# Optimization experiments

Measured on AMD Instinct MI355X. Metric: run time of the kernel, lower is better.

## Reference

```python
import jax, jax.numpy as jnp
import numpy as np

INPUT, HIDDEN, OUTPUT, LAYERS = 256, 512, 256, 2


def _lstm_cell(x, h, c, Wih, Whh, bih, bhh):
    # gates in torch order: i, f, g, o  -> [B, 4H]
    g = x @ Wih.T + bih + h @ Whh.T + bhh
    i, f, gg, o = jnp.split(g, 4, axis=-1)
    c_new = jax.nn.sigmoid(f) * c + jax.nn.sigmoid(i) * jnp.tanh(gg)
    h_new = jax.nn.sigmoid(o) * jnp.tanh(c_new)
    return h_new, c_new


def setup_inputs() -> dict:
    key = jax.random.key(0)
    ks = jax.random.split(key, 16)
    s = 0.05
    inp = {
        "z0": jax.random.normal(ks[0], (1024, INPUT), jnp.float32),
        "h0": jax.random.normal(ks[1], (LAYERS, 1024, HIDDEN), jnp.float32),
        "c0": jax.random.normal(ks[2], (LAYERS, 1024, HIDDEN), jnp.float32),
        # layer 0: input_size -> hidden
        "W_ih0": jax.random.normal(ks[3], (4 * HIDDEN, INPUT), jnp.float32) * s,
        "W_hh0": jax.random.normal(ks[4], (4 * HIDDEN, HIDDEN), jnp.float32) * s,
        "b_ih0": jax.random.normal(ks[5], (4 * HIDDEN,), jnp.float32) * s,
        "b_hh0": jax.random.normal(ks[6], (4 * HIDDEN,), jnp.float32) * s,
        # layer 1: hidden -> hidden
        "W_ih1": jax.random.normal(ks[7], (4 * HIDDEN, HIDDEN), jnp.float32) * s,
        "W_hh1": jax.random.normal(ks[8], (4 * HIDDEN, HIDDEN), jnp.float32) * s,
        "b_ih1": jax.random.normal(ks[9], (4 * HIDDEN,), jnp.float32) * s,
        "b_hh1": jax.random.normal(ks[10], (4 * HIDDEN,), jnp.float32) * s,
        # fc: hidden -> input (feedback), linear: input -> output
        "fc_W": jax.random.normal(ks[11], (INPUT, HIDDEN), jnp.float32) * s,
        "fc_b": jax.random.normal(ks[12], (INPUT,), jnp.float32) * s,
        "lin_W": jax.random.normal(ks[13], (OUTPUT, INPUT), jnp.float32) * s,
        "lin_b": jax.random.normal(ks[14], (OUTPUT,), jnp.float32) * s,
        "T2": 128,
    }
    return inp


def reference(z0, h0, c0, W_ih0, W_hh0, b_ih0, b_hh0,
              W_ih1, W_hh1, b_ih1, b_hh1, fc_W, fc_b, lin_W, lin_b, T2):
    params = [(W_ih0, W_hh0, b_ih0, b_hh0), (W_ih1, W_hh1, b_ih1, b_hh1)]

    def step(carry, _):
        z, h, c = carry          # z:[B,in], h/c:[L,B,H]
        x = z
        hs, cs = [], []
        for l, (Wih, Whh, bih, bhh) in enumerate(params):
            hn, cn = _lstm_cell(x, h[l], c[l], Wih, Whh, bih, bhh)
            hs.append(hn); cs.append(cn)
            x = hn
        z_new = x @ fc_W.T + fc_b
        return (z_new, jnp.stack(hs), jnp.stack(cs)), z_new

    _, zs = jax.lax.scan(step, (z0, h0, c0), None, length=T2)  # [T2,B,in]
    return zs @ lin_W.T + lin_b  # [T2, B, output]
```

## Files before the change

kernel.cpp:

```cpp
#include <hip/hip_runtime.h>


typedef __attribute__((ext_vector_type(8))) __bf16 bf16x8;
typedef __attribute__((ext_vector_type(16))) float f32x16;
typedef unsigned long long ull;

__device__ __forceinline__ f32x16 mfma_bf16(bf16x8 a, bf16x8 b, f32x16 c) {
  return __builtin_amdgcn_mfma_f32_32x32x16_bf16(a, b, c, 0, 0, 0);
}

__device__ __forceinline__ short f2bf(float f) {
  unsigned u = __float_as_uint(f);
  u += 0x7fffu + ((u >> 16) & 1u);
  return (short)(u >> 16);
}

__device__ __forceinline__ float sigm(float x) { return 1.0f / (1.0f + __expf(-x)); }
__device__ __forceinline__ float tanh_fast(float x) { return 2.0f / (1.0f + __expf(-2.0f * x)) - 1.0f; }

__device__ __forceinline__ f32x16 zero16() {
  f32x16 z;
#pragma unroll
  for (int i = 0; i < 16; ++i) z[i] = 0.0f;
  return z;
}

__device__ __forceinline__ void dma16(const void* g, void* l) {
  __builtin_amdgcn_global_load_lds(
      (const __attribute__((address_space(1))) void*)g,
      (__attribute__((address_space(3))) void*)l, 16, 0, 0);
}

#define AT_STRIDE 132

__global__ __launch_bounds__(256) void prep_kernel(
    const float* __restrict__ z0, const float* __restrict__ h0in,
    const float* __restrict__ Wih0, const float* __restrict__ Whh0,
    const float* __restrict__ bih0, const float* __restrict__ bhh0,
    const float* __restrict__ Wih1, const float* __restrict__ Whh1,
    const float* __restrict__ bih1, const float* __restrict__ bhh1,
    const float* __restrict__ fcW, const float* __restrict__ linW,
    short* __restrict__ wsw0, short* __restrict__ wsw1,
    short* __restrict__ fcWsw, short* __restrict__ linWsw,
    float* __restrict__ bias0, float* __restrict__ bias1,
    short* __restrict__ zb1, short* __restrict__ h0b0, short* __restrict__ h1b0,
    int* __restrict__ flags)
{
  int idx = blockIdx.x * 256 + threadIdx.x;
  if (idx < 1572864) {
    int jj = idx & 7, l = (idx >> 3) & 63, gg = (idx >> 9) & 3;
    int rest = idx >> 11;
    int s = rest % 48, b = rest / 48;
    int row = gg * 512 + b * 32 + (l & 31);
    int k = s * 16 + (l >> 5) * 8 + jj;
    wsw0[idx] = f2bf(k < 256 ? Wih0[row * 256 + k] : Whh0[row * 512 + (k - 256)]);
    return;
  }
  idx -= 1572864;
  if (idx < 2097152) {
    int jj = idx & 7, l = (idx >> 3) & 63, gg = (idx >> 9) & 3;
    int rest = idx >> 11;
    int s = rest & 63, b = rest >> 6;
    int row = gg * 512 + b * 32 + (l & 31);
    int k = s * 16 + (l >> 5) * 8 + jj;
    wsw1[idx] = f2bf(k < 512 ? Wih1[row * 512 + k] : Whh1[row * 512 + (k - 512)]);
    return;
  }
  idx -= 2097152;
  if (idx < 131072) {
    int jj = idx & 7, l = (idx >> 3) & 63, s = (idx >> 9) & 31, jz = idx >> 14;
    int col = jz * 32 + (l & 31);
    int k = s * 16 + (l >> 5) * 8 + jj;
    fcWsw[idx] = f2bf(fcW[col * 512 + k]);
    return;
  }
  idx -= 131072;
  if (idx < 65536) {
    int jj = idx & 7, l = (idx >> 3) & 63, s = (idx >> 9) & 15, jo = idx >> 13;
    int col = jo * 32 + (l & 31);
    int k = s * 16 + (l >> 5) * 8 + jj;
    linWsw[idx] = f2bf(linW[col * 256 + k]);
    return;
  }
  idx -= 65536;
  if (idx < 2048) { bias0[idx] = bih0[idx] + bhh0[idx]; return; }
  idx -= 2048;
  if (idx < 2048) { bias1[idx] = bih1[idx] + bhh1[idx]; return; }
  idx -= 2048;
  if (idx < 262144) { zb1[idx] = f2bf(z0[idx]); return; }
  idx -= 262144;
  if (idx < 524288) { h0b0[idx] = f2bf(h0in[idx]); return; }
  idx -= 524288;
  if (idx < 524288) { h1b0[idx] = f2bf(h0in[524288 + idx]); return; }
  idx -= 524288;
  if (idx < 8448) {
    int v = 0;
    if (idx < 8192) {
      int off = idx & 255;
      if (off == 32) v = 8;
      else if (off == 64 || off == 128) v = 16;
    }
    flags[idx] = v;
    return;
  }
}

__device__ __forceinline__ void wait1(int* c0, int v0) {
  __syncthreads();
  if (threadIdx.x == 0) {
    while (__hip_atomic_load(c0, __ATOMIC_RELAXED, __HIP_MEMORY_SCOPE_AGENT) < v0)
      __builtin_amdgcn_s_sleep(2);
    asm volatile("buffer_inv" ::: "memory");
  }
  __syncthreads();
}

__device__ __forceinline__ void wait2(int* c0, int v0, int* c1, int v1) {
  __syncthreads();
  if (threadIdx.x == 0) {
    while (__hip_atomic_load(c0, __ATOMIC_RELAXED, __HIP_MEMORY_SCOPE_AGENT) < v0 ||
           __hip_atomic_load(c1, __ATOMIC_RELAXED, __HIP_MEMORY_SCOPE_AGENT) < v1)
      __builtin_amdgcn_s_sleep(2);
    asm volatile("buffer_inv" ::: "memory");
  }
  __syncthreads();
}

__device__ __forceinline__ void produce(int* c) {
  asm volatile("s_waitcnt vmcnt(0)" ::: "memory");
  __syncthreads();
  if (threadIdx.x == 0)
    __hip_atomic_fetch_add(c, 1, __ATOMIC_RELAXED, __HIP_MEMORY_SCOPE_AGENT);
}

__device__ __forceinline__ void cell_warm(short* Bl, const short* __restrict__ wgl) {
  __syncthreads();
  const int t = threadIdx.x, w = t >> 6;
#pragma unroll
  for (int g = 0; g < 5; ++g)
#pragma unroll
    for (int i = 0; i < 2; ++i)
      dma16(wgl + (size_t)g * 8192 + (i * 512 + t) * 8,
            Bl + g * 8192 + i * 4096 + w * 512);
}

template <int NG, int TAG>
__device__ __forceinline__ void cell_phase_dma(
    short* Al, short* Bl, float* gbuf,
    const short* __restrict__ srcA, int ldA,
    const short* __restrict__ srcB, int ldB,
    const short* __restrict__ wgl,
    const float* __restrict__ bias,
    float* cr, short* hout, int row0, int j0)
{
  const int t = threadIdx.x;
  const int w = t >> 6, l = t & 63;
  const int gq = w >> 1, mh = w & 1;
  const int ln = l & 31, kh = l >> 5;

  auto issueA = [&](int g) {
    const short* asrc; int ald, gk;
    if (g < TAG) { asrc = srcA; ald = ldA; gk = g * 64; }
    else         { asrc = srcB; ald = ldB; gk = (g - TAG) * 64; }
    const short* gp = asrc + (size_t)(row0 + l) * ald + gk + w * 8;
    dma16(gp, Al + (g % 3) * 4096 + w * 512);
  };
  auto issueB = [&](int g) {
    const short* gb = wgl + (size_t)g * 8192;
    short* lb = Bl + (g % 5) * 8192;
#pragma unroll
    for (int i = 0; i < 2; ++i)
      dma16(gb + (i * 512 + t) * 8, lb + i * 4096 + w * 512);
  };

  f32x16 acc = zero16();
  issueA(0); issueA(1); issueA(2);

#pragma unroll
  for (int g = 0; g < NG; ++g) {
    if (g == 0)          asm volatile("s_waitcnt vmcnt(2)" ::: "memory");
    else if (g == 1)     asm volatile("s_waitcnt vmcnt(4)" ::: "memory");
    else if (g == 2)     asm volatile("s_waitcnt vmcnt(6)" ::: "memory");
    else if (g + 4 < NG) asm volatile("s_waitcnt vmcnt(8)" ::: "memory");
    else if (g + 3 < NG) asm volatile("s_waitcnt vmcnt(6)" ::: "memory");
    else if (g + 2 < NG) asm volatile("s_waitcnt vmcnt(4)" ::: "memory");
    else if (g + 1 < NG) asm volatile("s_waitcnt vmcnt(1)" ::: "memory");
    else                 asm volatile("s_waitcnt vmcnt(0)" ::: "memory");
    __builtin_amdgcn_s_barrier();
    __builtin_amdgcn_sched_barrier(0);
    const short* al = Al + (g % 3) * 4096;
    const short* bl = Bl + (g % 5) * 8192;
#pragma unroll
    for (int u = 0; u < 4; ++u) {
      bf16x8 a = *(const bf16x8*)&al[((u * 2 + kh) * 64 + mh * 32 + ln) * 8];
      bf16x8 b = *(const bf16x8*)&bl[((u * 4 + gq) * 64 + l) * 8];
      acc = mfma_bf16(a, b, acc);
    }
    __builtin_amdgcn_sched_barrier(0);
    __builtin_amdgcn_s_barrier();
    __builtin_amdgcn_sched_barrier(0);
    if (g + 3 < NG) issueA(g + 3);
    if (g + 5 < NG) issueB(g + 5);
  }

#pragma unroll
  for (int r = 0; r < 16; ++r) {
    int mloc = (r & 3) + 8 * (r >> 2) + 4 * kh + mh * 32;
    gbuf[(gq * 64 + mloc) * 32 + ln] = acc[r];
  }
  __syncthreads();
  const int m = t >> 3, nb = (t & 7) * 4;
  short hh[4];
#pragma unroll
  for (int u = 0; u < 4; ++u) {
    int n = nb + u, jn = j0 + n;
    float gi = gbuf[(0 * 64 + m) * 32 + n] + bias[jn];
    float gf = gbuf[(1 * 64 + m) * 32 + n] + bias[512 + jn];
    float gg = gbuf[(2 * 64 + m) * 32 + n] + bias[1024 + jn];
    float go = gbuf[(3 * 64 + m) * 32 + n] + bias[1536 + jn];
    float cn = sigm(gf) * cr[u] + sigm(gi) * tanh_fast(gg);
    cr[u] = cn;
    hh[u] = f2bf(sigm(go) * tanh_fast(cn));
  }
  ull hv; __builtin_memcpy(&hv, hh, 8);
  *(ull*)&hout[(size_t)(row0 + m) * 512 + j0 + nb] = hv;
}

template <int NQ>
__device__ __forceinline__ void proj_partials(
    short* At0, float* gbuf,
    const short* __restrict__ src, int ld,
    const short* __restrict__ wblk, int row0)
{
  const int t = threadIdx.x;
  const int w = t >> 6, l = t & 63;
  const int kq = w >> 1, mh = w & 1;
  const int ln = l & 31, kh = l >> 5;
  const int sks = t & 15, sm = t >> 4;
  f32x16 acc = zero16();
  uint4 pre[NQ][2];
#pragma unroll
  for (int q = 0; q < NQ; ++q)
#pragma unroll
    for (int i = 0; i < 2; ++i)
      pre[q][i] = *(const uint4*)&src[(row0 + sm + 32 * i) * ld + q * 128 + sks * 8];
#pragma unroll
  for (int q = 0; q < NQ; ++q) {
    __syncthreads();
#pragma unroll
    for (int i = 0; i < 2; ++i)
      *(uint4*)&At0[(sm + 32 * i) * AT_STRIDE + sks * 8] = pre[q][i];
    __syncthreads();
#pragma unroll
    for (int sl = 0; sl < 2; ++sl) {
      int s16 = kq * 2 + sl;
      bf16x8 a = *(const bf16x8*)&At0[(mh * 32 + ln) * AT_STRIDE + (s16 * 2 + kh) * 8];
      bf16x8 b = *(const bf16x8*)&wblk[((q * 8 + s16) * 64 + l) * 8];
      acc = mfma_bf16(a, b, acc);
    }
  }
  __syncthreads();
#pragma unroll
  for (int r = 0; r < 16; ++r) {
    int mloc = (r & 3) + 8 * (r >> 2) + 4 * kh + mh * 32;
    gbuf[(kq * 64 + mloc) * 32 + ln] = acc[r];
  }
  __syncthreads();
}

__global__ __launch_bounds__(512, 1) void decoder_persist(
    const short* __restrict__ wsw0, const short* __restrict__ wsw1,
    const short* __restrict__ fcWsw, const short* __restrict__ linWsw,
    const float* __restrict__ bias0, const float* __restrict__ bias1,
    const float* __restrict__ fcb, const float* __restrict__ linb,
    const float* __restrict__ c0in,
    short* h0x, short* h0y, short* h1x, short* h1y, short* zx, short* zy,
    int* flags, float* __restrict__ outp)
{
  __shared__ __align__(16) short Al[12288];
  __shared__ __align__(16) short Bl[40960];
  __shared__ int sgj[2];
  float* gbuf = (float*)Bl;
  short* Atp = Bl;
  float* gbufp = (float*)(Bl + 8448);

  if (threadIdx.x == 0) {
    unsigned xcc;
    asm volatile("s_getreg_b32 %0, hwreg(HW_REG_XCC_ID, 0, 32)" : "=s"(xcc));
    xcc &= 7u;
    int slot = __hip_atomic_fetch_add(&flags[8192 + (int)xcc * 32], 1,
                                      __ATOMIC_RELAXED, __HIP_MEMORY_SCOPE_AGENT);
    slot &= 31;
    sgj[0] = (int)xcc * 2 + (slot >> 4);
    sgj[1] = slot & 15;
  }
  __syncthreads();
  const int g = sgj[0], j = sgj[1];
  const int row0 = g * 64, j0 = j * 32;
  int* cnt = &flags[g * 256];
#define CZ(i)  (cnt + (0 + (i)) * 32)
#define CH0(i) (cnt + (2 + (i)) * 32)
#define CH1(i) (cnt + (4 + (i)) * 32)

  float c0r[4], c1r[4];
  {
    const int m = threadIdx.x >> 3, nb = (threadIdx.x & 7) * 4;
#pragma unroll
    for (int u = 0; u < 4; ++u) {
      c0r[u] = c0in[(size_t)(row0 + m) * 512 + j0 + nb + u];
      c1r[u] = c0in[524288 + (size_t)(row0 + m) * 512 + j0 + nb + u];
    }
  }

  short* h0buf[2] = {h0x, h0y};
  short* h1buf[2] = {h1x, h1y};
  short* zbuf[2] = {zx, zy};
  const short* wg0 = wsw0 + j * 98304;
  const short* wg1 = wsw1 + j * 131072;
  const short* wpj = (j < 8) ? (fcWsw + j * 16384) : (linWsw + (j - 8) * 8192);

#pragma unroll 1
  for (int t = 0; t < 128; ++t) {
    const int p = t & 1;
    const int half = (t >> 1) + 1;
    const int full = (t + 3) >> 1;
    cell_warm(Bl, wg0);
    wait2(CZ(p ^ 1), 8 * half, CH0(p), 16 * half);
    cell_phase_dma<12, 4>(Al, Bl, gbuf, zbuf[p ^ 1], 256, h0buf[p], 512,
                          wg0, bias0, c0r, h0buf[p ^ 1], row0, j0);
    produce(CH0(p ^ 1));
    cell_warm(Bl, wg1);
    wait2(CH0(p ^ 1), 16 * full, CH1(p), 16 * half);
    cell_phase_dma<16, 8>(Al, Bl, gbuf, h0buf[p ^ 1], 512, h1buf[p], 512,
                          wg1, bias1, c1r, h1buf[p ^ 1], row0, j0);
    produce(CH1(p ^ 1));
    if (j < 8) {
      wait1(CH1(p ^ 1), 16 * full);
      proj_partials<4>(Atp, gbufp, h1buf[p ^ 1], 512, wpj, row0);
      const int m = threadIdx.x >> 3, nb = (threadIdx.x & 7) * 4;
      const int n0 = j * 32;
      short zz[4];
#pragma unroll
      for (int u = 0; u < 4; ++u) {
        int n = nb + u;
        float v = gbufp[(0 * 64 + m) * 32 + n] + gbufp[(1 * 64 + m) * 32 + n] +
                  gbufp[(2 * 64 + m) * 32 + n] + gbufp[(3 * 64 + m) * 32 + n] +
                  fcb[n0 + n];
        zz[u] = f2bf(v);
      }
      ull zv; __builtin_memcpy(&zv, zz, 8);
      *(ull*)&zbuf[p][(size_t)(row0 + m) * 256 + n0 + nb] = zv;
      produce(CZ(p));
    } else if (t > 0) {
      proj_partials<2>(Atp, gbufp, zbuf[p ^ 1], 256, wpj, row0);
      const int m = threadIdx.x >> 3, nb = (threadIdx.x & 7) * 4;
      const int n0 = (j - 8) * 32;
      float4 ov;
      float* po = &ov.x;
#pragma unroll
      for (int u = 0; u < 4; ++u) {
        int n = nb + u;
        po[u] = gbufp[(0 * 64 + m) * 32 + n] + gbufp[(1 * 64 + m) * 32 + n] +
                gbufp[(2 * 64 + m) * 32 + n] + gbufp[(3 * 64 + m) * 32 + n] +
                linb[n0 + n];
      }
      *(float4*)&outp[(size_t)(t - 1) * 262144 + (size_t)(row0 + m) * 256 + n0 + nb] = ov;
    }
  }
  if (j >= 8) {
    wait1(CZ(1), 8 * 65);
    proj_partials<2>(Atp, gbufp, zbuf[1], 256, wpj, row0);
    const int m = threadIdx.x >> 3, nb = (threadIdx.x & 7) * 4;
    const int n0 = (j - 8) * 32;
    float4 ov;
    float* po = &ov.x;
#pragma unroll
    for (int u = 0; u < 4; ++u) {
      int n = nb + u;
      po[u] = gbufp[(0 * 64 + m) * 32 + n] + gbufp[(1 * 64 + m) * 32 + n] +
              gbufp[(2 * 64 + m) * 32 + n] + gbufp[(3 * 64 + m) * 32 + n] +
              linb[n0 + n];
    }
    *(float4*)&outp[(size_t)127 * 262144 + (size_t)(row0 + m) * 256 + n0 + nb] = ov;
  }
#undef CZ
#undef CH0
#undef CH1
}

extern "C" void kernel_launch(void* const* d_in, const int* in_sizes, int n_in,
                              void* d_out, int out_size, void* d_ws, size_t ws_size,
                              hipStream_t stream) {
  const float* z0   = (const float*)d_in[0];
  const float* h0in = (const float*)d_in[1];
  const float* c0in = (const float*)d_in[2];
  const float* Wih0 = (const float*)d_in[3];
  const float* Whh0 = (const float*)d_in[4];
  const float* bih0 = (const float*)d_in[5];
  const float* bhh0 = (const float*)d_in[6];
  const float* Wih1 = (const float*)d_in[7];
  const float* Whh1 = (const float*)d_in[8];
  const float* bih1 = (const float*)d_in[9];
  const float* bhh1 = (const float*)d_in[10];
  const float* fcW  = (const float*)d_in[11];
  const float* fcb  = (const float*)d_in[12];
  const float* linW = (const float*)d_in[13];
  const float* linb = (const float*)d_in[14];
  float* out = (float*)d_out;

  char* ws = (char*)d_ws;
  short* wsw0  = (short*)(ws + 0);
  short* wsw1  = (short*)(ws + 3145728);
  short* fcWsw = (short*)(ws + 7340032);
  short* linWsw= (short*)(ws + 7602176);
  float* bias0 = (float*)(ws + 7733248);
  float* bias1 = (float*)(ws + 7741440);
  short* zb0   = (short*)(ws + 7749632);
  short* zb1   = (short*)(ws + 8273920);
  short* h0b0  = (short*)(ws + 8798208);
  short* h0b1  = (short*)(ws + 9846784);
  short* h1b0  = (short*)(ws + 10895360);
  short* h1b1  = (short*)(ws + 11943936);
  int*   flags = (int*)  (ws + 12992512);

  prep_kernel<<<20273, 256, 0, stream>>>(z0, h0in, Wih0, Whh0, bih0, bhh0,
                                         Wih1, Whh1, bih1, bhh1, fcW, linW,
                                         wsw0, wsw1, fcWsw, linWsw, bias0, bias1,
                                         zb1, h0b0, h1b0, flags);

  decoder_persist<<<256, 512, 0, stream>>>(
      wsw0, wsw1, fcWsw, linWsw, bias0, bias1, fcb, linb, c0in,
      h0b0, h0b1, h1b0, h1b1, zb0, zb1, flags, out);
}
```

Measured before the change: 4.820 ms.

## Reorder K to put recurrent state first and prefetch it before the cross-block wait

Swaps the weight packing so the recurrent hidden-state K range comes before the input range. The first three A tiles, which depend only on the block's own previous h, can then be DMA'd before waiting on the other blocks' flags. The weight ring deepens from 5 to 6 stages and LDS grows to match. Biases are hoisted into registers and projection weights are preloaded into registers. This hides latency on the serial recurrence critical path, at the cost of more LDS and registers and trickier vmcnt bookkeeping.

```diff
diff --git a/kernel.cpp b/kernel.cpp
--- a/kernel.cpp
+++ b/kernel.cpp
@@ -53,7 +53,7 @@
     int s = rest % 48, b = rest / 48;
     int row = gg * 512 + b * 32 + (l & 31);
     int k = s * 16 + (l >> 5) * 8 + jj;
-    wsw0[idx] = f2bf(k < 256 ? Wih0[row * 256 + k] : Whh0[row * 512 + (k - 256)]);
+    wsw0[idx] = f2bf(k < 512 ? Whh0[row * 512 + k] : Wih0[row * 256 + (k - 512)]);
     return;
   }
   idx -= 1572864;
@@ -63,7 +63,7 @@
     int s = rest & 63, b = rest >> 6;
     int row = gg * 512 + b * 32 + (l & 31);
     int k = s * 16 + (l >> 5) * 8 + jj;
-    wsw1[idx] = f2bf(k < 512 ? Wih1[row * 512 + k] : Whh1[row * 512 + (k - 512)]);
+    wsw1[idx] = f2bf(k < 512 ? Whh1[row * 512 + k] : Wih1[row * 512 + (k - 512)]);
     return;
   }
   idx -= 2097152;
@@ -137,11 +137,20 @@
   __syncthreads();
   const int t = threadIdx.x, w = t >> 6;
 #pragma unroll
-  for (int g = 0; g < 5; ++g)
+  for (int g = 0; g < 6; ++g)
 #pragma unroll
     for (int i = 0; i < 2; ++i)
       dma16(wgl + (size_t)g * 8192 + (i * 512 + t) * 8,
             Bl + g * 8192 + i * 4096 + w * 512);
+}
+
+__device__ __forceinline__ void proA3(short* Al, const short* __restrict__ srcA,
+                                      int ldA, int row0) {
+  const int t = threadIdx.x, w = t >> 6, l = t & 63;
+#pragma unroll
+  for (int g = 0; g < 3; ++g)
+    dma16(srcA + (size_t)(row0 + l) * ldA + g * 64 + w * 8,
+          Al + g * 4096 + w * 512);
 }
 
 template <int NG, int TAG>
@@ -150,7 +159,7 @@
     const short* __restrict__ srcA, int ldA,
     const short* __restrict__ srcB, int ldB,
     const short* __restrict__ wgl,
-    const float* __restrict__ bias,
+    const float (&br)[4][4],
     float* cr, short* hout, int row0, int j0)
 {
   const int t = threadIdx.x;
@@ -167,29 +176,29 @@
   };
   auto issueB = [&](int g) {
     const short* gb = wgl + (size_t)g * 8192;
-    short* lb = Bl + (g % 5) * 8192;
+    short* lb = Bl + (g % 6) * 8192;
 #pragma unroll
     for (int i = 0; i < 2; ++i)
       dma16(gb + (i * 512 + t) * 8, lb + i * 4096 + w * 512);
   };
 
   f32x16 acc = zero16();
-  issueA(0); issueA(1); issueA(2);
 
 #pragma unroll
   for (int g = 0; g < NG; ++g) {
-    if (g == 0)          asm volatile("s_waitcnt vmcnt(2)" ::: "memory");
-    else if (g == 1)     asm volatile("s_waitcnt vmcnt(4)" ::: "memory");
-    else if (g == 2)     asm volatile("s_waitcnt vmcnt(6)" ::: "memory");
-    else if (g + 4 < NG) asm volatile("s_waitcnt vmcnt(8)" ::: "memory");
-    else if (g + 3 < NG) asm volatile("s_waitcnt vmcnt(6)" ::: "memory");
-    else if (g + 2 < NG) asm volatile("s_waitcnt vmcnt(4)" ::: "memory");
-    else if (g + 1 < NG) asm volatile("s_waitcnt vmcnt(1)" ::: "memory");
-    else                 asm volatile("s_waitcnt vmcnt(0)" ::: "memory");
+    if (g == 0)           asm volatile("s_waitcnt vmcnt(2)" ::: "memory");
+    else if (g == 1)      asm volatile("s_waitcnt vmcnt(4)" ::: "memory");
+    else if (g == 2)      asm volatile("s_waitcnt vmcnt(6)" ::: "memory");
+    else if (g + 6 <= NG) asm volatile("s_waitcnt vmcnt(8)" ::: "memory");
+    else if (g + 5 == NG) asm volatile("s_waitcnt vmcnt(6)" ::: "memory");
+    else if (g + 4 == NG) asm volatile("s_waitcnt vmcnt(4)" ::: "memory");
+    else if (g + 3 == NG) asm volatile("s_waitcnt vmcnt(2)" ::: "memory");
+    else if (g + 2 == NG) asm volatile("s_waitcnt vmcnt(1)" ::: "memory");
+    else                  asm volatile("s_waitcnt vmcnt(0)" ::: "memory");
     __builtin_amdgcn_s_barrier();
     __builtin_amdgcn_sched_barrier(0);
     const short* al = Al + (g % 3) * 4096;
-    const short* bl = Bl + (g % 5) * 8192;
+    const short* bl = Bl + (g % 6) * 8192;
 #pragma unroll
     for (int u = 0; u < 4; ++u) {
       bf16x8 a = *(const bf16x8*)&al[((u * 2 + kh) * 64 + mh * 32 + ln) * 8];
@@ -200,7 +209,7 @@
     __builtin_amdgcn_s_barrier();
     __builtin_amdgcn_sched_barrier(0);
     if (g + 3 < NG) issueA(g + 3);
-    if (g + 5 < NG) issueB(g + 5);
+    if (g + 6 < NG) issueB(g + 6);
   }
 
 #pragma unroll
@@ -213,11 +222,11 @@
   short hh[4];
 #pragma unroll
   for (int u = 0; u < 4; ++u) {
-    int n = nb + u, jn = j0 + n;
-    float gi = gbuf[(0 * 64 + m) * 32 + n] + bias[jn];
-    float gf = gbuf[(1 * 64 + m) * 32 + n] + bias[512 + jn];
-    float gg = gbuf[(2 * 64 + m) * 32 + n] + bias[1024 + jn];
-    float go = gbuf[(3 * 64 + m) * 32 + n] + bias[1536 + jn];
+    int n = nb + u;
+    float gi = gbuf[(0 * 64 + m) * 32 + n] + br[0][u];
+    float gf = gbuf[(1 * 64 + m) * 32 + n] + br[1][u];
+    float gg = gbuf[(2 * 64 + m) * 32 + n] + br[2][u];
+    float go = gbuf[(3 * 64 + m) * 32 + n] + br[3][u];
     float cn = sigm(gf) * cr[u] + sigm(gi) * tanh_fast(gg);
     cr[u] = cn;
     hh[u] = f2bf(sigm(go) * tanh_fast(cn));
@@ -239,11 +248,16 @@
   const int sks = t & 15, sm = t >> 4;
   f32x16 acc = zero16();
   uint4 pre[NQ][2];
-#pragma unroll
-  for (int q = 0; q < NQ; ++q)
+  bf16x8 bfr[NQ][2];
+#pragma unroll
+  for (int q = 0; q < NQ; ++q) {
 #pragma unroll
     for (int i = 0; i < 2; ++i)
       pre[q][i] = *(const uint4*)&src[(row0 + sm + 32 * i) * ld + q * 128 + sks * 8];
+#pragma unroll
+    for (int sl = 0; sl < 2; ++sl)
+      bfr[q][sl] = *(const bf16x8*)&wblk[((q * 8 + kq * 2 + sl) * 64 + l) * 8];
+  }
 #pragma unroll
   for (int q = 0; q < NQ; ++q) {
     __syncthreads();
@@ -255,8 +269,7 @@
     for (int sl = 0; sl < 2; ++sl) {
       int s16 = kq * 2 + sl;
       bf16x8 a = *(const bf16x8*)&At0[(mh * 32 + ln) * AT_STRIDE + (s16 * 2 + kh) * 8];
-      bf16x8 b = *(const bf16x8*)&wblk[((q * 8 + s16) * 64 + l) * 8];
-      acc = mfma_bf16(a, b, acc);
+      acc = mfma_bf16(a, bfr[q][sl], acc);
     }
   }
   __syncthreads();
@@ -278,7 +291,7 @@
     int* flags, float* __restrict__ outp)
 {
   __shared__ __align__(16) short Al[12288];
-  __shared__ __align__(16) short Bl[40960];
+  __shared__ __align__(16) short Bl[49152];
   __shared__ int sgj[2];
   float* gbuf = (float*)Bl;
   short* Atp = Bl;
@@ -302,13 +315,20 @@
 #define CH0(i) (cnt + (2 + (i)) * 32)
 #define CH1(i) (cnt + (4 + (i)) * 32)
 
-  float c0r[4], c1r[4];
+  float c0r[4], c1r[4], b0r[4][4], b1r[4][4], fbr[4];
   {
     const int m = threadIdx.x >> 3, nb = (threadIdx.x & 7) * 4;
 #pragma unroll
     for (int u = 0; u < 4; ++u) {
       c0r[u] = c0in[(size_t)(row0 + m) * 512 + j0 + nb + u];
       c1r[u] = c0in[524288 + (size_t)(row0 + m) * 512 + j0 + nb + u];
+      int jn = j0 + nb + u;
+#pragma unroll
+      for (int gt = 0; gt < 4; ++gt) {
+        b0r[gt][u] = bias0[gt * 512 + jn];
+        b1r[gt][u] = bias1[gt * 512 + jn];
+      }
+      fbr[u] = (j < 8) ? fcb[j * 32 + nb + u] : linb[(j - 8) * 32 + nb + u];
     }
   }
 
@@ -325,14 +345,21 @@
     const int half = (t >> 1) + 1;
     const int full = (t + 3) >> 1;
     cell_warm(Bl, wg0);
+    proA3(Al, h0buf[p], 512, row0);
     wait2(CZ(p ^ 1), 8 * half, CH0(p), 16 * half);
-    cell_phase_dma<12, 4>(Al, Bl, gbuf, zbuf[p ^ 1], 256, h0buf[p], 512,
-                          wg0, bias0, c0r, h0buf[p ^ 1], row0, j0);
+    cell_phase_dma<12, 8>(Al, Bl, gbuf, h0buf[p], 512, zbuf[p ^ 1], 256,
+                          wg0, b0r, c0r, h0buf[p ^ 1], row0, j0);
     produce(CH0(p ^ 1));
     cell_warm(Bl, wg1);
-    wait2(CH0(p ^ 1), 16 * full, CH1(p), 16 * half);
-    cell_phase_dma<16, 8>(Al, Bl, gbuf, h0buf[p ^ 1], 512, h1buf[p], 512,
-                          wg1, bias1, c1r, h1buf[p ^ 1], row0, j0);
+    if (j < 8) {
+      proA3(Al, h1buf[p], 512, row0);
+      wait2(CH0(p ^ 1), 16 * full, CH1(p), 16 * half);
+    } else {
+      wait2(CH0(p ^ 1), 16 * full, CH1(p), 16 * half);
+      proA3(Al, h1buf[p], 512, row0);
+    }
+    cell_phase_dma<16, 8>(Al, Bl, gbuf, h1buf[p], 512, h0buf[p ^ 1], 512,
+                          wg1, b1r, c1r, h1buf[p ^ 1], row0, j0);
     produce(CH1(p ^ 1));
     if (j < 8) {
       wait1(CH1(p ^ 1), 16 * full);
@@ -345,7 +372,7 @@
         int n = nb + u;
         float v = gbufp[(0 * 64 + m) * 32 + n] + gbufp[(1 * 64 + m) * 32 + n] +
                   gbufp[(2 * 64 + m) * 32 + n] + gbufp[(3 * 64 + m) * 32 + n] +
-                  fcb[n0 + n];
+                  fbr[u];
         zz[u] = f2bf(v);
       }
       ull zv; __builtin_memcpy(&zv, zz, 8);
@@ -362,7 +389,7 @@
         int n = nb + u;
         po[u] = gbufp[(0 * 64 + m) * 32 + n] + gbufp[(1 * 64 + m) * 32 + n] +
                 gbufp[(2 * 64 + m) * 32 + n] + gbufp[(3 * 64 + m) * 32 + n] +
-                linb[n0 + n];
+                fbr[u];
       }
       *(float4*)&outp[(size_t)(t - 1) * 262144 + (size_t)(row0 + m) * 256 + n0 + nb] = ov;
     }
@@ -379,7 +406,7 @@
       int n = nb + u;
       po[u] = gbufp[(0 * 64 + m) * 32 + n] + gbufp[(1 * 64 + m) * 32 + n] +
               gbufp[(2 * 64 + m) * 32 + n] + gbufp[(3 * 64 + m) * 32 + n] +
-              linb[n0 + n];
+              fbr[u];
     }
     *(float4*)&outp[(size_t)127 * 262144 + (size_t)(row0 + m) * 256 + n0 + nb] = ov;
   }
```

After: 4.845 ms. About the same (+0.5%).
